# Performance work log

Hardware: AMD Instinct MI355X
Metric: run time of the kernel (lower is better)

The kernel has to match this reference:

```python
import jax, jax.numpy as jnp
import numpy as np

B, T, D, H, K, V = 2, 2048, 2048, 16, 128, 128


def _causal_conv(x, w):
    # x: [B,T,H,C], w: [H,C,4] -> depthwise causal conv, kernel size 4
    t = x.shape[1]
    xp = jnp.pad(x, ((0, 0), (3, 0), (0, 0), (0, 0)))
    return sum(xp[:, i:i + t] * w[:, :, i] for i in range(4))


def _l2norm(x):
    return x / jnp.maximum(jnp.linalg.norm(x, axis=-1, keepdims=True), 1e-12)


def _kda_scan(q, k, v, g, beta):
    # q,k: [B,T,H,K]; v: [B,T,H,V]; g: [B,T,H,K]; beta: [B,T,H]
    b, t, h, kd = q.shape
    vd = v.shape[-1]

    def step(S, inp):
        qt, kt, vt, gt, bt = inp
        S = S * jnp.exp(gt)[..., None]                       # per-key-channel decay
        err = vt - jnp.einsum('bhk,bhkv->bhv', kt, S)        # delta-rule error
        S = S + bt[..., None, None] * (kt[..., :, None] * err[..., None, :])
        ot = jnp.einsum('bhk,bhkv->bhv', qt, S)
        return S, ot

    tm = lambda a: jnp.moveaxis(a, 1, 0)
    S0 = jnp.zeros((b, h, kd, vd), q.dtype)
    _, ys = jax.lax.scan(step, S0, (tm(q), tm(k), tm(v), tm(g), tm(beta)))
    return jnp.moveaxis(ys, 0, 1)


def setup_inputs() -> dict:
    key = jax.random.key(0)
    ks = jax.random.split(key, 16)
    s = 0.02
    rng = np.random.default_rng(0)
    dt = np.exp(rng.uniform(size=H * K) * (np.log(0.1) - np.log(0.001)) + np.log(0.001)).clip(min=1e-4)
    dt_bias = (dt + np.log(-np.expm1(-dt))).astype(np.float32)
    A_log = np.log(rng.uniform(1.0, 16.0, size=H)).astype(np.float32)
    return {
        'x': jax.random.normal(ks[0], (B, T, D), jnp.float32),
        'Wq': jax.random.normal(ks[1], (H * K, D), jnp.float32) * s,
        'Wk': jax.random.normal(ks[2], (H * K, D), jnp.float32) * s,
        'Wv': jax.random.normal(ks[3], (H * V, D), jnp.float32) * s,
        'Wf1': jax.random.normal(ks[4], (V, D), jnp.float32) * s,
        'Wf2': jax.random.normal(ks[5], (H * K, V), jnp.float32) * s,
        'Wb': jax.random.normal(ks[6], (H, D), jnp.float32) * s,
        'Wg1': jax.random.normal(ks[7], (V, D), jnp.float32) * s,
        'Wg2': jax.random.normal(ks[8], (H * V, V), jnp.float32) * s,
        'bg': jnp.zeros((H * V,), jnp.float32),
        'o_norm_w': jnp.ones((V,), jnp.float32),
        'Wout': jax.random.normal(ks[9], (D, H * V), jnp.float32) * s,
        'A_log': jnp.asarray(A_log),
        'dt_bias': jnp.asarray(dt_bias),
        'qcw': jax.random.normal(ks[10], (H, K, 4), jnp.float32) * 0.1,
        'kcw': jax.random.normal(ks[11], (H, K, 4), jnp.float32) * 0.1,
        'vcw': jax.random.normal(ks[12], (H, V, 4), jnp.float32) * 0.1,
    }


def reference(x, Wq, Wk, Wv, Wf1, Wf2, Wb, Wg1, Wg2, bg, o_norm_w, Wout, A_log, dt_bias, qcw, kcw, vcw):
    b, t, d = x.shape
    h, kd = qcw.shape[0], qcw.shape[1]
    vd = vcw.shape[1]
    q = (x @ Wq.T).reshape(b, t, h, kd)
    k = (x @ Wk.T).reshape(b, t, h, kd)
    v = (x @ Wv.T).reshape(b, t, h, vd)
    q = _l2norm(jax.nn.silu(_causal_conv(q, qcw)))
    k = _l2norm(jax.nn.silu(_causal_conv(k, kcw)))
    v = jax.nn.silu(_causal_conv(v, vcw))
    g_raw = ((x @ Wf1.T) @ Wf2.T).reshape(b, t, h, kd)
    g = -jnp.exp(A_log)[None, None, :, None] * jax.nn.softplus(g_raw + dt_bias.reshape(h, kd))
    beta = jax.nn.sigmoid(x @ Wb.T)  # [B,T,H]
    y = _kda_scan(q, k, v, g, beta)  # [B,T,H,V]
    gate = ((x @ Wg1.T) @ Wg2.T + bg).reshape(b, t, h, vd)
    eps = 1.1920929e-07  # torch.finfo(float32).eps (F.rms_norm default)
    y = y * jax.lax.rsqrt(jnp.mean(y * y, axis=-1, keepdims=True) + eps) * o_norm_w
    y = y * jax.nn.sigmoid(gate)
    return y.reshape(b, t, h * vd) @ Wout.T
```

## Files before the change

kernel.cpp:

```cpp
#include <hip/hip_runtime.h>

typedef unsigned short u16;
typedef unsigned int u32;

using short8 = __attribute__((ext_vector_type(8))) short;
using f32x4  = __attribute__((ext_vector_type(4))) float;

constexpr int kB = 2, kT = 2048, kD = 2048, kH = 16, kK = 128, kV = 128;
constexpr int kM  = kB * kT;
constexpr int kHK = kH * kK;
constexpr int kHV = kH * kV;
constexpr int CC  = 16;
constexpr int NCH = kT / CC;

constexpr size_t OFF_XB    = 0;
constexpr size_t OFF_WQKV  = 16777216;
constexpr size_t OFF_QC    = 0;
constexpr size_t OFF_YF    = 0;
constexpr size_t OFF_WF1B  = 41943040;
constexpr size_t OFF_WG1B  = 42467328;
constexpr size_t OFF_WBP   = 42991616;
constexpr size_t OFF_WF2B  = 43515904;
constexpr size_t OFF_WG2B  = 44040192;
constexpr size_t OFF_FGB   = 44564480;
constexpr size_t OFF_QKVR  = 48758784;
constexpr size_t OFF_QHB   = 48758784;
constexpr size_t OFF_KBB   = 65536000;
constexpr size_t OFF_KHB   = 82313216;
constexpr size_t OFF_YGB   = 82313216;
constexpr size_t OFF_GRAW  = 99090432;
constexpr size_t OFF_LAM   = 99090432;
constexpr size_t OFF_WINV  = 101187584;
constexpr size_t OFF_MM    = 105381888;
constexpr size_t OFF_GATEB = 115867648;
constexpr size_t OFF_WOUTB = 132644864;
constexpr size_t OFF_KC    = 141033472;
constexpr size_t OFF_VT    = 174587904;
constexpr size_t OFF_GK    = 208142336;
constexpr size_t OFF_BETA  = 241696768;

__device__ __forceinline__ u16 f2bf(float f) {
  union { float f; u32 u; } a; a.f = f;
  u32 u = a.u;
  u += 0x7fffu + ((u >> 16) & 1u);
  return (u16)(u >> 16);
}
__device__ __forceinline__ float bflo(u32 u) {
  union { u32 u; float f; } a; a.u = u << 16; return a.f;
}
__device__ __forceinline__ float bfhi(u32 u) {
  union { u32 u; float f; } a; a.u = u & 0xffff0000u; return a.f;
}
__device__ __forceinline__ float sigmoidf(float x) { return 1.0f / (1.0f + expf(-x)); }

#define GL_AS1 __attribute__((address_space(1)))
#define GL_AS3 __attribute__((address_space(3)))
__device__ __forceinline__ void async_lds16(const void* g, void* l) {
  __builtin_amdgcn_global_load_lds((GL_AS1 u32*)(size_t)g,
                                   (GL_AS3 u32*)(u32)(size_t)l, 16, 0, 0);
}

__global__ __launch_bounds__(256) void cast_all(
    const float* __restrict__ x, const float* __restrict__ Wq,
    const float* __restrict__ Wk, const float* __restrict__ Wv,
    const float* __restrict__ Wout, const float* __restrict__ Wf1,
    const float* __restrict__ Wg1, const float* __restrict__ Wf2,
    const float* __restrict__ Wg2,
    u16* __restrict__ xb, u16* __restrict__ wqkv, u16* __restrict__ woutb,
    u16* __restrict__ wf1b, u16* __restrict__ wg1b, u16* __restrict__ wf2b,
    u16* __restrict__ wg2b) {
  long qi = (long)blockIdx.x * 256 + threadIdx.x;
  const float* src; u16* dst; long off;
  if (qi < 2097152)      { src = x;    dst = xb;             off = qi; }
  else if (qi < 3145728) { src = Wq;   dst = wqkv;           off = qi - 2097152; }
  else if (qi < 4194304) { src = Wk;   dst = wqkv + 4194304; off = qi - 3145728; }
  else if (qi < 5242880) { src = Wv;   dst = wqkv + 8388608; off = qi - 4194304; }
  else if (qi < 6291456) { src = Wout; dst = woutb;          off = qi - 5242880; }
  else if (qi < 6356992) { src = Wf1;  dst = wf1b;           off = qi - 6291456; }
  else if (qi < 6422528) { src = Wg1;  dst = wg1b;           off = qi - 6356992; }
  else if (qi < 6488064) { src = Wf2;  dst = wf2b;           off = qi - 6422528; }
  else                   { src = Wg2;  dst = wg2b;           off = qi - 6488064; }
  long i = off * 4;
  float4 v = *(const float4*)(src + i);
  uint2 st;
  st.x = (u32)f2bf(v.x) | ((u32)f2bf(v.y) << 16);
  st.y = (u32)f2bf(v.z) | ((u32)f2bf(v.w) << 16);
  *(uint2*)(dst + i) = st;
}

__global__ __launch_bounds__(256) void pad_wb(const float* __restrict__ Wb,
                                              u16* __restrict__ out) {
  int i = (blockIdx.x * 256 + threadIdx.x) * 4;
  int row = i >> 11;
  uint2 st; st.x = 0; st.y = 0;
  if (row < 16) {
    float4 v = *(const float4*)(Wb + i);
    st.x = (u32)f2bf(v.x) | ((u32)f2bf(v.y) << 16);
    st.y = (u32)f2bf(v.z) | ((u32)f2bf(v.w) << 16);
  }
  *(uint2*)(out + i) = st;
}

template <bool BF16OUT>
__global__ __launch_bounds__(256) void gemm_bt(const u16* __restrict__ A,
                                               const u16* __restrict__ B,
                                               void* __restrict__ Cout,
                                               int lda, int ldb, int ldc, int K) {
  __shared__ u16 As[128 * 32];
  __shared__ u16 Bs[128 * 32];
  const int tid  = threadIdx.x;
  const int lane = tid & 63;
  const int wave = tid >> 6;
  const int wm = (wave >> 1) * 64;
  const int wn = (wave & 1) * 64;
  const long row0 = (long)blockIdx.x * 128;
  const long col0 = (long)blockIdx.y * 128;
  const int srow = tid >> 2;
  const int scol = (tid & 3) * 8;
  const u16* aptr = A + (row0 + srow) * (size_t)lda + scol;
  const u16* bptr = B + (col0 + srow) * (size_t)ldb + scol;
  u16* asd  = &As[tid * 8];
  u16* asd2 = &As[2048 + tid * 8];
  u16* bsd  = &Bs[tid * 8];
  u16* bsd2 = &Bs[2048 + tid * 8];
  const int mrow = lane & 15;
  const int kq = (lane >> 4) * 8;
  f32x4 acc[4][4] = {};
  for (int k0 = 0; k0 < K; k0 += 32) {
    async_lds16(aptr, asd);
    async_lds16(aptr + (size_t)64 * lda, asd2);
    async_lds16(bptr, bsd);
    async_lds16(bptr + (size_t)64 * ldb, bsd2);
    aptr += 32; bptr += 32;
    __syncthreads();
    short8 af[4], bfr[4];
#pragma unroll
    for (int i = 0; i < 4; ++i)
      af[i] = *(const short8*)(&As[(wm + i * 16 + mrow) * 32 + kq]);
#pragma unroll
    for (int j = 0; j < 4; ++j)
      bfr[j] = *(const short8*)(&Bs[(wn + j * 16 + mrow) * 32 + kq]);
#pragma unroll
    for (int i = 0; i < 4; ++i)
#pragma unroll
      for (int j = 0; j < 4; ++j)
        acc[i][j] = __builtin_amdgcn_mfma_f32_16x16x32_bf16(af[i], bfr[j], acc[i][j], 0, 0, 0);
    __syncthreads();
  }
  const int cn = lane & 15;
  const int rq = (lane >> 4) * 4;
#pragma unroll
  for (int i = 0; i < 4; ++i)
#pragma unroll
    for (int j = 0; j < 4; ++j) {
      size_t r = (size_t)(row0 + wm + i * 16 + rq);
      size_t c = (size_t)(col0 + wn + j * 16 + cn);
#pragma unroll
      for (int rr = 0; rr < 4; ++rr) {
        if constexpr (BF16OUT)
          ((u16*)Cout)[(r + rr) * ldc + c] = f2bf(acc[i][j][rr]);
        else
          ((float*)Cout)[(r + rr) * ldc + c] = acc[i][j][rr];
      }
    }
}

__global__ __launch_bounds__(256) void convprep(
    const u16* __restrict__ qkv, const u16* __restrict__ graw,
    const u16* __restrict__ fgb,
    const float* __restrict__ qcw, const float* __restrict__ kcw,
    const float* __restrict__ vcw, const float* __restrict__ A_log,
    const float* __restrict__ dt_bias,
    float* __restrict__ qc, float* __restrict__ kc, float* __restrict__ vt,
    float* __restrict__ gdec, float* __restrict__ beta) {
  const int wid  = blockIdx.x * 4 + (threadIdx.x >> 6);
  const int lane = threadIdx.x & 63;
  const int h  = wid & 15;
  const int bt = wid >> 4;
  const int t  = bt & (kT - 1);
  const int b  = bt >> 11;
  const int c0 = lane * 2;
  const size_t colofs = (size_t)h * kK + c0;
  const size_t rowb = (size_t)bt * 6144 + colofs;
  const float* wq = qcw + colofs * 4;
  const float* wk = kcw + colofs * 4;
  const float* wv = vcw + colofs * 4;
  float qa0 = 0, qa1 = 0, ka0 = 0, ka1 = 0, va0 = 0, va1 = 0;
#pragma unroll
  for (int i = 0; i < 4; ++i) {
    int tt = t - 3 + i;
    if (tt >= 0) {
      size_t ro = rowb - (size_t)(3 - i) * 6144;
      u32 uq = *(const u32*)(qkv + ro);
      u32 uk = *(const u32*)(qkv + ro + 2048);
      u32 uv = *(const u32*)(qkv + ro + 4096);
      qa0 += bflo(uq) * wq[i];  qa1 += bfhi(uq) * wq[4 + i];
      ka0 += bflo(uk) * wk[i];  ka1 += bfhi(uk) * wk[4 + i];
      va0 += bflo(uv) * wv[i];  va1 += bfhi(uv) * wv[4 + i];
    }
  }
  qa0 *= sigmoidf(qa0); qa1 *= sigmoidf(qa1);
  ka0 *= sigmoidf(ka0); ka1 *= sigmoidf(ka1);
  va0 *= sigmoidf(va0); va1 *= sigmoidf(va1);
  float sq = qa0 * qa0 + qa1 * qa1;
  float sk = ka0 * ka0 + ka1 * ka1;
#pragma unroll
  for (int m = 1; m < 64; m <<= 1) {
    sq += __shfl_xor(sq, m);
    sk += __shfl_xor(sk, m);
  }
  float qinv = 1.0f / fmaxf(sqrtf(sq), 1e-12f);
  float kinv = 1.0f / fmaxf(sqrtf(sk), 1e-12f);
  const int bh = b * kH + h;
  const size_t outb = ((size_t)bh * kT + t) * kK + c0;
  *(float2*)(qc + outb) = make_float2(qa0 * qinv, qa1 * qinv);
  *(float2*)(kc + outb) = make_float2(ka0 * kinv, ka1 * kinv);
  const size_t vtb = ((size_t)(bh * 8 + (c0 >> 4)) * kT + t) * 16 + (c0 & 15);
  *(float2*)(vt + vtb) = make_float2(va0, va1);
  u32 ug = *(const u32*)(graw + (size_t)bt * kHK + colofs);
  float Ae = expf(A_log[h]);
  float g0 = bflo(ug) + dt_bias[colofs];
  float g1 = bfhi(ug) + dt_bias[colofs + 1];
  float sp0 = (g0 > 15.f) ? g0 : log1pf(expf(g0));
  float sp1 = (g1 > 15.f) ? g1 : log1pf(expf(g1));
  *(float2*)(gdec + outb) = make_float2(-Ae * sp0, -Ae * sp1);
  if (lane == 0) {
    float bv = bflo((u32)fgb[(size_t)bt * 384 + 256 + h]);
    beta[(size_t)bh * kT + t] = sigmoidf(bv);
  }
}

__global__ __launch_bounds__(256) void kda_p1(
    const float* __restrict__ qc, const float* __restrict__ kc,
    const float* __restrict__ gk, const float* __restrict__ betap,
    u16* __restrict__ qhb, u16* __restrict__ khb, u16* __restrict__ kbb,
    float* __restrict__ lamC, float* __restrict__ winv,
    float* __restrict__ mmat) {
  __shared__ float kL[CC][132], qL[CC][132], gL[CC][132];
  __shared__ float As[CC][CC], Ms[CC][CC];
  __shared__ float bet[CC];
  const int tid = threadIdx.x;
  const int bh = blockIdx.x >> 7;
  const int ch = blockIdx.x & 127;
  const size_t base = ((size_t)bh * kT + ch * CC) * kK;
  const int e = tid * 8;
  const int t = e >> 7, k = e & 127;
  {
    *(float4*)&kL[t][k]     = *(const float4*)(kc + base + e);
    *(float4*)&kL[t][k + 4] = *(const float4*)(kc + base + e + 4);
    *(float4*)&qL[t][k]     = *(const float4*)(qc + base + e);
    *(float4*)&qL[t][k + 4] = *(const float4*)(qc + base + e + 4);
    *(float4*)&gL[t][k]     = *(const float4*)(gk + base + e);
    *(float4*)&gL[t][k + 4] = *(const float4*)(gk + base + e + 4);
    if (tid < CC) bet[tid] = betap[(size_t)bh * kT + ch * CC + tid];
  }
  __syncthreads();
  if (tid < kK) {
    float a = gL[0][tid];
#pragma unroll
    for (int tt = 1; tt < CC; ++tt) { a += gL[tt][tid]; gL[tt][tid] = a; }
  }
  __syncthreads();
  float khr[8], qhr[8], kbw[8];
  u32 pk[4] = {0,0,0,0}, pq[4] = {0,0,0,0}, pb[4] = {0,0,0,0};
#pragma unroll
  for (int j = 0; j < 8; ++j) {
    float G  = gL[t][k + j];
    float GC = gL[CC - 1][k + j];
    float eg = __expf(G);
    float kh = kL[t][k + j] * eg;
    float qh = qL[t][k + j] * eg;
    float kb = kL[t][k + j] * __expf(GC - G);
    u16 a = f2bf(kh), b_ = f2bf(qh), c = f2bf(kb);
    pk[j >> 1] |= ((u32)a)  << (16 * (j & 1));
    pq[j >> 1] |= ((u32)b_) << (16 * (j & 1));
    pb[j >> 1] |= ((u32)c)  << (16 * (j & 1));
    khr[j] = bflo(a);
    qhr[j] = bflo(b_);
    kbw[j] = bflo(c) * __expf(-GC);
  }
  *(uint4*)(khb + base + e) = *(uint4*)pk;
  *(uint4*)(qhb + base + e) = *(uint4*)pq;
  *(uint4*)(kbb + base + e) = *(uint4*)pb;
  if (tid < kK)
    lamC[((size_t)bh * NCH + ch) * kK + tid] = __expf(gL[CC - 1][tid]);
  __syncthreads();
#pragma unroll
  for (int j = 0; j < 8; ++j) {
    kL[t][k + j] = khr[j];
    qL[t][k + j] = qhr[j];
    gL[t][k + j] = kbw[j];
  }
  __syncthreads();
  {
    const int t2 = tid >> 4, s = tid & 15;
    float av = 0.f, mv = 0.f;
    for (int kk = 0; kk < kK; ++kk) {
      float w = gL[s][kk];
      av = fmaf(kL[t2][kk], w, av);
      mv = fmaf(qL[t2][kk], w, mv);
    }
    As[t2][s] = (s < t2)  ? av : 0.f;
    Ms[t2][s] = (s <= t2) ? mv : 0.f;
  }
  __syncthreads();
  if (tid < CC) {
    const int s = tid;
    float x[CC];
#pragma unroll
    for (int tt = 0; tt < CC; ++tt) {
      float sum = 0.f;
      for (int r = 0; r < tt; ++r) sum += As[tt][r] * x[r];
      x[tt] = ((tt == s) ? bet[tt] : 0.f) - bet[tt] * sum;
    }
    const size_t wb = ((size_t)bh * NCH + ch) * 256;
#pragma unroll
    for (int tt = 0; tt < CC; ++tt) winv[wb + tt * 16 + s] = x[tt];
  }
  mmat[((size_t)bh * NCH + ch) * 256 + tid] = Ms[tid >> 4][tid & 15];
}

__global__ __launch_bounds__(256) void kda_p2(
    const u16* __restrict__ khb, const u16* __restrict__ qhb,
    const u16* __restrict__ kbb, const float* __restrict__ lamC,
    const float* __restrict__ winv, const float* __restrict__ mmat,
    const float* __restrict__ vt, float* __restrict__ yf) {
  __shared__ u16 khs[2][CC][136];
  __shared__ u16 qhs[2][CC][136];
  __shared__ u16 kbs[2][kK][40];
  __shared__ float vsx[2][CC][17];
  __shared__ float wsx[2][CC][16];
  __shared__ float msx[2][CC][16];
  __shared__ float lamx[2][kK];
  __shared__ u16 s0h[CC][136];
  __shared__ u16 s0l[CC][136];
  __shared__ float pd[4][CC][17];
  __shared__ float qd[4][CC][17];
  __shared__ float t1r[CC][17];
  __shared__ float ufx[CC][17];
  __shared__ u16 ush[CC][40];
  __shared__ u16 usl[CC][40];
  const int tid = threadIdx.x;
  const int w = tid >> 6, lane = tid & 63;
  const int m15 = lane & 15, q = lane >> 4, q8 = q * 8;
  const int t_ = tid >> 4, v_ = tid & 15;
  const int blk = blockIdx.x;
  const int bh = (blk & 7) + ((blk >> 6) << 3);
  const int vs = (blk >> 3) & 7;
  const int cb = vs * 16;
  for (int i = tid; i < CC * 136 / 2; i += 256) { ((u32*)s0h)[i] = 0; ((u32*)s0l)[i] = 0; }
  for (int i = tid; i < 2 * kK * 40 / 2; i += 256) ((u32*)kbs)[i] = 0;
  for (int i = tid; i < CC * 40 / 2; i += 256) { ((u32*)ush)[i] = 0; ((u32*)usl)[i] = 0; }

  uint4 rkh, rqh, rkb; float rv, rw, rm, rl;
  auto loadCh = [&](int ch) {
    const size_t cbase = ((size_t)bh * kT + ch * CC) * kK;
    rkh = *(const uint4*)(khb + cbase + tid * 8);
    rqh = *(const uint4*)(qhb + cbase + tid * 8);
    rkb = *(const uint4*)(kbb + cbase + tid * 8);
    rv  = vt[((size_t)(bh * 8 + vs) * kT + ch * CC) * 16 + tid];
    const size_t sm = (size_t)bh * NCH + ch;
    rw  = winv[sm * 256 + tid];
    rm  = mmat[sm * 256 + tid];
    rl  = (tid < kK) ? lamC[sm * kK + tid] : 0.f;
  };
  auto writeStage = [&](int b) {
    const int tr = tid >> 4, tc = (tid & 15) * 8;
    *(uint4*)&khs[b][tr][tc] = rkh;
    *(uint4*)&qhs[b][tr][tc] = rqh;
    u16 kv[8]; *(uint4*)kv = rkb;
#pragma unroll
    for (int j = 0; j < 8; ++j) kbs[b][tc + j][tr] = kv[j];
    vsx[b][tr][tid & 15] = rv;
    wsx[b][tr][tid & 15] = rw;
    msx[b][tr][tid & 15] = rm;
    if (tid < kK) lamx[b][tid] = rl;
  };

  f32x4 St[2] = {};
  loadCh(0);
  for (int ch = 0; ch < NCH; ++ch) {
    const int b = ch & 1;
    writeStage(b);
    if (ch + 1 < NCH) loadCh(ch + 1);
    __syncthreads();
    short8 aK = *(const short8*)&khs[b][m15][w * 32 + q8];
    short8 aQ = *(const short8*)&qhs[b][m15][w * 32 + q8];
    short8 sH = *(const short8*)&s0h[m15][w * 32 + q8];
    short8 sL = *(const short8*)&s0l[m15][w * 32 + q8];
    f32x4 z = {0.f, 0.f, 0.f, 0.f};
    f32x4 P  = __builtin_amdgcn_mfma_f32_16x16x32_bf16(aK, sL, z, 0, 0, 0);
    P        = __builtin_amdgcn_mfma_f32_16x16x32_bf16(aK, sH, P, 0, 0, 0);
    f32x4 Qp = __builtin_amdgcn_mfma_f32_16x16x32_bf16(aQ, sL, z, 0, 0, 0);
    Qp       = __builtin_amdgcn_mfma_f32_16x16x32_bf16(aQ, sH, Qp, 0, 0, 0);
#pragma unroll
    for (int r = 0; r < 4; ++r) {
      pd[w][q * 4 + r][m15] = P[r];
      qd[w][q * 4 + r][m15] = Qp[r];
    }
    __syncthreads();
    float t1 = vsx[b][t_][v_] -
               ((pd[0][t_][v_] + pd[1][t_][v_]) + (pd[2][t_][v_] + pd[3][t_][v_]));
    float qs = (qd[0][t_][v_] + qd[1][t_][v_]) + (qd[2][t_][v_] + qd[3][t_][v_]);
    t1r[t_][v_] = t1;
    __syncthreads();
    float u = 0.f;
#pragma unroll
    for (int s = 0; s < CC; ++s) u = fmaf(wsx[b][t_][s], t1r[s][v_], u);
    ufx[t_][v_] = u;
    u16 uh = f2bf(u);
    ush[v_][t_] = uh;
    usl[v_][t_] = f2bf(u - bflo(uh));
    __syncthreads();
    float o = qs;
#pragma unroll
    for (int s = 0; s < CC; ++s) o = fmaf(msx[b][t_][s], ufx[s][v_], o);
    yf[((size_t)bh * kT + ch * CC + t_) * kV + cb + v_] = o;
    short8 bH = *(const short8*)&ush[m15][q8];
    short8 bL = *(const short8*)&usl[m15][q8];
#pragma unroll
    for (int j = 0; j < 2; ++j) {
      const int kt = w * 32 + j * 16;
      f32x4 S = St[j];
#pragma unroll
      for (int r = 0; r < 4; ++r) S[r] *= lamx[b][kt + q * 4 + r];
      short8 aB = *(const short8*)&kbs[b][kt + m15][q8];
      S = __builtin_amdgcn_mfma_f32_16x16x32_bf16(aB, bL, S, 0, 0, 0);
      S = __builtin_amdgcn_mfma_f32_16x16x32_bf16(aB, bH, S, 0, 0, 0);
      St[j] = S;
      u16 h0 = f2bf(S[0]), h1 = f2bf(S[1]), h2 = f2bf(S[2]), h3 = f2bf(S[3]);
      uint2 hw; hw.x = (u32)h0 | ((u32)h1 << 16); hw.y = (u32)h2 | ((u32)h3 << 16);
      *(uint2*)&s0h[m15][kt + q * 4] = hw;
      uint2 lw;
      lw.x = (u32)f2bf(S[0] - bflo(h0)) | ((u32)f2bf(S[1] - bflo(h1)) << 16);
      lw.y = (u32)f2bf(S[2] - bflo(h2)) | ((u32)f2bf(S[3] - bflo(h3)) << 16);
      *(uint2*)&s0l[m15][kt + q * 4] = lw;
    }
  }
}

__global__ __launch_bounds__(256) void postk(
    const float* __restrict__ yf, const u16* __restrict__ gateb,
    const float* __restrict__ bg, const float* __restrict__ onw,
    u16* __restrict__ ygb) {
  const int wid  = blockIdx.x * 4 + (threadIdx.x >> 6);
  const int lane = threadIdx.x & 63;
  const int h  = wid & 15;
  const int bt = wid >> 4;
  const int t  = bt & (kT - 1);
  const int b  = bt >> 11;
  const int v0 = lane * 2;
  const size_t yi = ((size_t)(b * kH + h) * kT + t) * kV + v0;
  float2 yv = *(const float2*)(yf + yi);
  float s = yv.x * yv.x + yv.y * yv.y;
#pragma unroll
  for (int m = 1; m < 64; m <<= 1) s += __shfl_xor(s, m);
  float scale = rsqrtf(s * (1.0f / 128.0f) + 1.1920929e-07f);
  const size_t gi = (size_t)bt * kHV + (size_t)h * kV + v0;
  u32 ug = *(const u32*)(gateb + gi);
  float g0 = bflo(ug) + bg[h * kV + v0];
  float g1 = bfhi(ug) + bg[h * kV + v0 + 1];
  float r0 = yv.x * scale * onw[v0] * sigmoidf(g0);
  float r1 = yv.y * scale * onw[v0 + 1] * sigmoidf(g1);
  *(u32*)(ygb + gi) = (u32)f2bf(r0) | ((u32)f2bf(r1) << 16);
}

extern "C" void kernel_launch(void* const* d_in, const int* in_sizes, int n_in,
                              void* d_out, int out_size, void* d_ws, size_t ws_size,
                              hipStream_t stream) {
  (void)in_sizes; (void)n_in; (void)out_size; (void)ws_size;
  const float* x    = (const float*)d_in[0];
  const float* Wq   = (const float*)d_in[1];
  const float* Wk   = (const float*)d_in[2];
  const float* Wv   = (const float*)d_in[3];
  const float* Wf1  = (const float*)d_in[4];
  const float* Wf2  = (const float*)d_in[5];
  const float* Wb   = (const float*)d_in[6];
  const float* Wg1  = (const float*)d_in[7];
  const float* Wg2  = (const float*)d_in[8];
  const float* bg   = (const float*)d_in[9];
  const float* onw  = (const float*)d_in[10];
  const float* Wout = (const float*)d_in[11];
  const float* A_log   = (const float*)d_in[12];
  const float* dt_bias = (const float*)d_in[13];
  const float* qcw  = (const float*)d_in[14];
  const float* kcw  = (const float*)d_in[15];
  const float* vcw  = (const float*)d_in[16];

  char* ws = (char*)d_ws;
  u16* xb     = (u16*)(ws + OFF_XB);
  u16* wqkv   = (u16*)(ws + OFF_WQKV);
  u16* wf1b   = (u16*)(ws + OFF_WF1B);
  u16* wg1b   = (u16*)(ws + OFF_WG1B);
  u16* wbp    = (u16*)(ws + OFF_WBP);
  u16* wf2b   = (u16*)(ws + OFF_WF2B);
  u16* wg2b   = (u16*)(ws + OFF_WG2B);
  u16* woutb  = (u16*)(ws + OFF_WOUTB);
  u16* fgb    = (u16*)(ws + OFF_FGB);
  u16* qkvraw = (u16*)(ws + OFF_QKVR);
  u16* graw   = (u16*)(ws + OFF_GRAW);
  u16* gateb  = (u16*)(ws + OFF_GATEB);
  u16* qhb    = (u16*)(ws + OFF_QHB);
  u16* khb    = (u16*)(ws + OFF_KHB);
  u16* kbb    = (u16*)(ws + OFF_KBB);
  u16* ygb    = (u16*)(ws + OFF_YGB);
  float* qcf   = (float*)(ws + OFF_QC);
  float* kcf   = (float*)(ws + OFF_KC);
  float* vtf   = (float*)(ws + OFF_VT);
  float* gkf   = (float*)(ws + OFF_GK);
  float* betaf = (float*)(ws + OFF_BETA);
  float* yff   = (float*)(ws + OFF_YF);
  float* lamf  = (float*)(ws + OFF_LAM);
  float* winvf = (float*)(ws + OFF_WINV);
  float* mmf   = (float*)(ws + OFF_MM);

  cast_all<<<25600, 256, 0, stream>>>(x, Wq, Wk, Wv, Wout, Wf1, Wg1, Wf2, Wg2,
                                      xb, wqkv, woutb, wf1b, wg1b, wf2b, wg2b);
  pad_wb<<<(128 * 2048 / 4 + 255) / 256, 256, 0, stream>>>(Wb, wbp);

  dim3 blk(256);
  gemm_bt<true><<<dim3(kM / 128, 6144 / 128), blk, 0, stream>>>(
      xb, wqkv, qkvraw, kD, kD, 6144, kD);
  gemm_bt<true><<<dim3(kM / 128, 384 / 128), blk, 0, stream>>>(
      xb, wf1b, fgb, kD, kD, 384, kD);
  gemm_bt<true><<<dim3(kM / 128, kHK / 128), blk, 0, stream>>>(
      fgb, wf2b, graw, 384, kV, kHK, kV);
  gemm_bt<true><<<dim3(kM / 128, kHV / 128), blk, 0, stream>>>(
      fgb + 128, wg2b, gateb, 384, kV, kHV, kV);

  convprep<<<kB * kT * kH / 4, 256, 0, stream>>>(qkvraw, graw, fgb,
                                                 qcw, kcw, vcw, A_log, dt_bias,
                                                 qcf, kcf, vtf, gkf, betaf);

  kda_p1<<<32 * NCH, 256, 0, stream>>>(qcf, kcf, gkf, betaf,
                                       qhb, khb, kbb, lamf, winvf, mmf);
  kda_p2<<<256, 256, 0, stream>>>(khb, qhb, kbb, lamf, winvf, mmf, vtf, yff);

  postk<<<kB * kT * kH / 4, 256, 0, stream>>>(yff, gateb, bg, onw, ygb);

  gemm_bt<false><<<dim3(kM / 128, kD / 128), blk, 0, stream>>>(
      ygb, woutb, (float*)d_out, kHV, kHV, kD, kHV);
}
```

Measured before the change: 841.0 us.

## Split KDA recurrence across 16 value slices and pre-transpose kb in p1

The chunked recurrence kernel now splits each head's value dimension into 16 slices of 8 columns instead of 8 slices of 16, doubling the grid to 512 blocks so more CUs work on the serial scan. The per-chunk kb matrix is written by p1 already transposed, letting p2 stage it with one vector store instead of scattered 16-bit LDS writes. The cost is that each block redoes the K·S MFMA work for only half as many useful value columns, and half the threads idle in the small scalar stages; the MFMA B operand now holds only 8 real columns padded with zeros.

```diff
diff --git a/kernel.cpp b/kernel.cpp
--- a/kernel.cpp
+++ b/kernel.cpp
@@ -233,7 +233,7 @@
 __global__ __launch_bounds__(256) void kda_p1(
     const float* __restrict__ qc, const float* __restrict__ kc,
     const float* __restrict__ gk, const float* __restrict__ betap,
-    u16* __restrict__ qhb, u16* __restrict__ khb, u16* __restrict__ kbb,
+    u16* __restrict__ qhb, u16* __restrict__ khb, u16* __restrict__ kbt,
     float* __restrict__ lamC, float* __restrict__ winv,
     float* __restrict__ mmat) {
   __shared__ float kL[CC][132], qL[CC][132], gL[CC][132];
@@ -262,7 +262,8 @@
   }
   __syncthreads();
   float khr[8], qhr[8], kbw[8];
-  u32 pk[4] = {0,0,0,0}, pq[4] = {0,0,0,0}, pb[4] = {0,0,0,0};
+  u16 kbv[8];
+  u32 pk[4] = {0,0,0,0}, pq[4] = {0,0,0,0};
 #pragma unroll
   for (int j = 0; j < 8; ++j) {
     float G  = gL[t][k + j];
@@ -274,14 +275,19 @@
     u16 a = f2bf(kh), b_ = f2bf(qh), c = f2bf(kb);
     pk[j >> 1] |= ((u32)a)  << (16 * (j & 1));
     pq[j >> 1] |= ((u32)b_) << (16 * (j & 1));
-    pb[j >> 1] |= ((u32)c)  << (16 * (j & 1));
+    kbv[j] = c;
     khr[j] = bflo(a);
     qhr[j] = bflo(b_);
-    kbw[j] = bflo(c) * __expf(-GC);
+    kbw[j] = bflo((u32)c) * __expf(-GC);
   }
   *(uint4*)(khb + base + e) = *(uint4*)pk;
   *(uint4*)(qhb + base + e) = *(uint4*)pq;
-  *(uint4*)(kbb + base + e) = *(uint4*)pb;
+  {
+    const size_t kb2 = ((size_t)bh * NCH + ch) * (size_t)(kK * CC) +
+                       (size_t)k * CC + t;
+#pragma unroll
+    for (int j = 0; j < 8; ++j) kbt[kb2 + (size_t)j * CC] = kbv[j];
+  }
   if (tid < kK)
     lamC[((size_t)bh * NCH + ch) * kK + tid] = __expf(gL[CC - 1][tid]);
   __syncthreads();
@@ -322,32 +328,31 @@
 
 __global__ __launch_bounds__(256) void kda_p2(
     const u16* __restrict__ khb, const u16* __restrict__ qhb,
-    const u16* __restrict__ kbb, const float* __restrict__ lamC,
+    const u16* __restrict__ kbt, const float* __restrict__ lamC,
     const float* __restrict__ winv, const float* __restrict__ mmat,
     const float* __restrict__ vt, float* __restrict__ yf) {
   __shared__ u16 khs[2][CC][136];
   __shared__ u16 qhs[2][CC][136];
   __shared__ u16 kbs[2][kK][40];
-  __shared__ float vsx[2][CC][17];
-  __shared__ float wsx[2][CC][16];
-  __shared__ float msx[2][CC][16];
+  __shared__ float vsx[2][CC][9];
+  __shared__ float wsx[2][CC][17];
+  __shared__ float msx[2][CC][17];
   __shared__ float lamx[2][kK];
   __shared__ u16 s0h[CC][136];
   __shared__ u16 s0l[CC][136];
   __shared__ float pd[4][CC][17];
   __shared__ float qd[4][CC][17];
-  __shared__ float t1r[CC][17];
-  __shared__ float ufx[CC][17];
+  __shared__ float t1r[CC][9];
+  __shared__ float ufx[CC][9];
   __shared__ u16 ush[CC][40];
   __shared__ u16 usl[CC][40];
   const int tid = threadIdx.x;
   const int w = tid >> 6, lane = tid & 63;
   const int m15 = lane & 15, q = lane >> 4, q8 = q * 8;
-  const int t_ = tid >> 4, v_ = tid & 15;
   const int blk = blockIdx.x;
-  const int bh = (blk & 7) + ((blk >> 6) << 3);
-  const int vs = (blk >> 3) & 7;
-  const int cb = vs * 16;
+  const int bh = (blk & 7) + ((blk >> 7) << 3);
+  const int vs = (blk >> 3) & 15;
+  const int cb = vs * 8;
   for (int i = tid; i < CC * 136 / 2; i += 256) { ((u32*)s0h)[i] = 0; ((u32*)s0l)[i] = 0; }
   for (int i = tid; i < 2 * kK * 40 / 2; i += 256) ((u32*)kbs)[i] = 0;
   for (int i = tid; i < CC * 40 / 2; i += 256) { ((u32*)ush)[i] = 0; ((u32*)usl)[i] = 0; }
@@ -357,8 +362,11 @@
     const size_t cbase = ((size_t)bh * kT + ch * CC) * kK;
     rkh = *(const uint4*)(khb + cbase + tid * 8);
     rqh = *(const uint4*)(qhb + cbase + tid * 8);
-    rkb = *(const uint4*)(kbb + cbase + tid * 8);
-    rv  = vt[((size_t)(bh * 8 + vs) * kT + ch * CC) * 16 + tid];
+    rkb = *(const uint4*)(kbt + ((size_t)bh * NCH + ch) * (size_t)(kK * CC) + tid * 8);
+    rv  = (tid < CC * 8)
+            ? vt[((size_t)(bh * 8 + (vs >> 1)) * kT + ch * CC + (tid >> 3)) * 16 +
+                 (vs & 1) * 8 + (tid & 7)]
+            : 0.f;
     const size_t sm = (size_t)bh * NCH + ch;
     rw  = winv[sm * 256 + tid];
     rm  = mmat[sm * 256 + tid];
@@ -368,10 +376,8 @@
     const int tr = tid >> 4, tc = (tid & 15) * 8;
     *(uint4*)&khs[b][tr][tc] = rkh;
     *(uint4*)&qhs[b][tr][tc] = rqh;
-    u16 kv[8]; *(uint4*)kv = rkb;
-#pragma unroll
-    for (int j = 0; j < 8; ++j) kbs[b][tc + j][tr] = kv[j];
-    vsx[b][tr][tid & 15] = rv;
+    *(uint4*)&kbs[b][tid >> 1][(tid & 1) * 8] = rkb;
+    if (tid < CC * 8) vsx[b][tid >> 3][tid & 7] = rv;
     wsx[b][tr][tid & 15] = rw;
     msx[b][tr][tid & 15] = rm;
     if (tid < kK) lamx[b][tid] = rl;
@@ -399,23 +405,31 @@
       qd[w][q * 4 + r][m15] = Qp[r];
     }
     __syncthreads();
-    float t1 = vsx[b][t_][v_] -
-               ((pd[0][t_][v_] + pd[1][t_][v_]) + (pd[2][t_][v_] + pd[3][t_][v_]));
-    float qs = (qd[0][t_][v_] + qd[1][t_][v_]) + (qd[2][t_][v_] + qd[3][t_][v_]);
-    t1r[t_][v_] = t1;
+    const int tt = tid >> 3, vv = tid & 7;
+    float qs = 0.f;
+    if (tid < 128) {
+      float t1 = vsx[b][tt][vv] -
+                 ((pd[0][tt][vv] + pd[1][tt][vv]) + (pd[2][tt][vv] + pd[3][tt][vv]));
+      qs = (qd[0][tt][vv] + qd[1][tt][vv]) + (qd[2][tt][vv] + qd[3][tt][vv]);
+      t1r[tt][vv] = t1;
+    }
     __syncthreads();
-    float u = 0.f;
-#pragma unroll
-    for (int s = 0; s < CC; ++s) u = fmaf(wsx[b][t_][s], t1r[s][v_], u);
-    ufx[t_][v_] = u;
-    u16 uh = f2bf(u);
-    ush[v_][t_] = uh;
-    usl[v_][t_] = f2bf(u - bflo(uh));
+    if (tid < 128) {
+      float u = 0.f;
+#pragma unroll
+      for (int s = 0; s < CC; ++s) u = fmaf(wsx[b][tt][s], t1r[s][vv], u);
+      ufx[tt][vv] = u;
+      u16 uh = f2bf(u);
+      ush[vv][tt] = uh;
+      usl[vv][tt] = f2bf(u - bflo(uh));
+    }
     __syncthreads();
-    float o = qs;
-#pragma unroll
-    for (int s = 0; s < CC; ++s) o = fmaf(msx[b][t_][s], ufx[s][v_], o);
-    yf[((size_t)bh * kT + ch * CC + t_) * kV + cb + v_] = o;
+    if (tid < 128) {
+      float o = qs;
+#pragma unroll
+      for (int s = 0; s < CC; ++s) o = fmaf(msx[b][tt][s], ufx[s][vv], o);
+      yf[((size_t)bh * kT + ch * CC + tt) * kV + cb + vv] = o;
+    }
     short8 bH = *(const short8*)&ush[m15][q8];
     short8 bL = *(const short8*)&usl[m15][q8];
 #pragma unroll
@@ -534,7 +548,7 @@
 
   kda_p1<<<32 * NCH, 256, 0, stream>>>(qcf, kcf, gkf, betaf,
                                        qhb, khb, kbb, lamf, winvf, mmf);
-  kda_p2<<<256, 256, 0, stream>>>(khb, qhb, kbb, lamf, winvf, mmf, vtf, yff);
+  kda_p2<<<512, 256, 0, stream>>>(khb, qhb, kbb, lamf, winvf, mmf, vtf, yff);
 
   postk<<<kB * kT * kH / 4, 256, 0, stream>>>(yff, gateb, bg, onw, ygb);
 
```

After: 808.0 us. 1.04x faster.
